# Performance work log

Measured on AMD Instinct MI355X. Metric: run time of the kernel, lower is better.

The kernel has to match this reference:

```python
import jax, jax.numpy as jnp
import numpy as np

NUM_NODES = 100_000
NUM_EDGES = 3_200_000
THETA = 1.0  # module hyperparameter (default 1.0)


def setup_inputs() -> dict:
    key = jax.random.key(0)
    k_v, k_src, k_dst, k_t1, k_t2, k_r = jax.random.split(key, 6)
    v = jax.random.normal(k_v, (NUM_NODES,), dtype=jnp.float32)
    src = jax.random.randint(k_src, (NUM_EDGES,), 0, NUM_NODES, dtype=jnp.int32)
    dst = jax.random.randint(k_dst, (NUM_EDGES,), 0, NUM_NODES, dtype=jnp.int32)
    theta_sd_1 = jax.random.normal(k_t1, (NUM_EDGES,), dtype=jnp.float32) * 0.1
    theta_sd_2 = jax.random.normal(k_t2, (NUM_EDGES,), dtype=jnp.float32) * 0.1
    # conductance = 1/resistance, resistance in (0.5, 2.0) -> conductance in (0.5, 2.0)
    conductance = 1.0 / jax.random.uniform(k_r, (NUM_EDGES,), dtype=jnp.float32, minval=0.5, maxval=2.0)
    return {"t": 0, "v": v, "src": src, "dst": dst,
            "theta_sd_1": theta_sd_1, "theta_sd_2": theta_sd_2,
            "conductance": conductance}


def reference(t, v, src, dst, theta_sd_1, theta_sd_2, conductance):
    # per-edge gated current: g(vs, vd) = relu(theta1*(vs - vd) + theta2)
    diff = v[src] - v[dst]                                   # [E]
    current = conductance * jax.nn.relu(theta_sd_1 * diff + theta_sd_2)  # [E]
    incoming = jax.ops.segment_sum(current, dst, num_segments=NUM_NODES)  # [N]
    outgoing = jax.ops.segment_sum(current, src, num_segments=NUM_NODES)  # [N]
    return (incoming - outgoing) / THETA
```

## Files before the change

kernel.cpp:

```cpp
#include <hip/hip_runtime.h>


#define RANGE   16384
#define P1_BLK  512

__global__ __launch_bounds__(256) void edge_current_kernel(
    const float* __restrict__ v,
    const int*   __restrict__ src,
    const int*   __restrict__ dst,
    const float* __restrict__ t1,
    const float* __restrict__ t2,
    const float* __restrict__ cond,
    float*       __restrict__ cur,
    int E)
{
    const int E4 = E & ~3;
    int i = (blockIdx.x * blockDim.x + threadIdx.x) * 4;
    int stride = gridDim.x * blockDim.x * 4;
    for (; i < E4; i += stride) {
        int4   s4 = *(const int4*)  (src  + i);
        int4   d4 = *(const int4*)  (dst  + i);
        float4 a4 = *(const float4*)(t1   + i);
        float4 b4 = *(const float4*)(t2   + i);
        float4 c4 = *(const float4*)(cond + i);
        float4 o;
        float x0 = fmaf(a4.x, v[s4.x] - v[d4.x], b4.x);
        float x1 = fmaf(a4.y, v[s4.y] - v[d4.y], b4.y);
        float x2 = fmaf(a4.z, v[s4.z] - v[d4.z], b4.z);
        float x3 = fmaf(a4.w, v[s4.w] - v[d4.w], b4.w);
        o.x = x0 > 0.0f ? c4.x * x0 : 0.0f;
        o.y = x1 > 0.0f ? c4.y * x1 : 0.0f;
        o.z = x2 > 0.0f ? c4.z * x2 : 0.0f;
        o.w = x3 > 0.0f ? c4.w * x3 : 0.0f;
        *(float4*)(cur + i) = o;
    }
    int t = E4 + blockIdx.x * blockDim.x + threadIdx.x;
    if (t < E) {
        float x = fmaf(t1[t], v[src[t]] - v[dst[t]], t2[t]);
        cur[t] = x > 0.0f ? cond[t] * x : 0.0f;
    }
}

__global__ __launch_bounds__(P1_BLK) void range_accum_kernel(
    const int*   __restrict__ src,
    const int*   __restrict__ dst,
    const float* __restrict__ cur,
    float*       __restrict__ partial,
    int N, int E, int B, int sliceLen)
{
    __shared__ __align__(16) float acc[RANGE];

    const int b    = blockIdx.x % B;
    const int r    = blockIdx.x / B;
    const int base = r * RANGE;
    const int len  = min(RANGE, N - base);

    for (int i = threadIdx.x; i < RANGE; i += P1_BLK) acc[i] = 0.0f;
    __syncthreads();

    const int E4 = E & ~3;
    const int s0 = b * sliceLen;
    const int s1 = min(s0 + sliceLen, E4);

    for (int i = s0 + threadIdx.x * 4; i < s1; i += P1_BLK * 4) {
        int4   ss = *(const int4*)  (src + i);
        int4   dd = *(const int4*)  (dst + i);
        float4 cc = *(const float4*)(cur + i);
        #define PROC(S, D, C)                                              \
            if ((C) != 0.0f) {                                             \
                unsigned du = (unsigned)((D) - base);                      \
                if (du < (unsigned)len) atomicAdd(&acc[du],  (C));         \
                unsigned su = (unsigned)((S) - base);                      \
                if (su < (unsigned)len) atomicAdd(&acc[su], -(C));         \
            }
        PROC(ss.x, dd.x, cc.x)
        PROC(ss.y, dd.y, cc.y)
        PROC(ss.z, dd.z, cc.z)
        PROC(ss.w, dd.w, cc.w)
    }
    if (b == B - 1) {
        for (int i = E4 + threadIdx.x; i < E; i += P1_BLK) {
            float c = cur[i];
            PROC(src[i], dst[i], c)
        }
        #undef PROC
    }

    __syncthreads();
    float* outp = partial + (size_t)b * N + base;
    const int len4 = len & ~3;
    for (int i = threadIdx.x * 4; i < len4; i += P1_BLK * 4)
        *(float4*)(outp + i) = *(const float4*)&acc[i];
    for (int i = len4 + threadIdx.x; i < len; i += P1_BLK)
        outp[i] = acc[i];
}

__global__ __launch_bounds__(256) void reduce_kernel(
    const float* __restrict__ partial, float* __restrict__ out, int N4, int B)
{
    int n = blockIdx.x * blockDim.x + threadIdx.x;
    if (n < N4) {
        float4 s = make_float4(0.f, 0.f, 0.f, 0.f);
        for (int p = 0; p < B; ++p) {
            float4 q = ((const float4*)partial)[(size_t)p * N4 + n];
            s.x += q.x; s.y += q.y; s.z += q.z; s.w += q.w;
        }
        ((float4*)out)[n] = s;
    }
}

__global__ __launch_bounds__(256) void atomic_fallback_kernel(
    const float* __restrict__ v, const int* __restrict__ src, const int* __restrict__ dst,
    const float* __restrict__ t1, const float* __restrict__ t2, const float* __restrict__ cond,
    float* __restrict__ out, int E)
{
    int i = blockIdx.x * blockDim.x + threadIdx.x;
    int stride = gridDim.x * blockDim.x;
    for (; i < E; i += stride) {
        int s = src[i], d = dst[i];
        float x = fmaf(t1[i], v[s] - v[d], t2[i]);
        if (x > 0.0f) {
            float c = cond[i] * x;
            atomicAdd(&out[d], c);
            atomicAdd(&out[s], -c);
        }
    }
}

extern "C" void kernel_launch(void* const* d_in, const int* in_sizes, int n_in,
                              void* d_out, int out_size, void* d_ws, size_t ws_size,
                              hipStream_t stream) {
    const float* v    = (const float*)d_in[1];
    const int*   src  = (const int*)  d_in[2];
    const int*   dst  = (const int*)  d_in[3];
    const float* t1   = (const float*)d_in[4];
    const float* t2   = (const float*)d_in[5];
    const float* cond = (const float*)d_in[6];
    float* out = (float*)d_out;
    const int E = in_sizes[2];
    const int N = out_size;

    const size_t curBytes = (((size_t)E * sizeof(float)) + 255) & ~(size_t)255;
    const size_t perCopy  = (size_t)N * sizeof(float);

    int B = 0;
    const int cands[] = {64, 48, 32, 24, 16, 12, 8};
    for (int c : cands) {
        if (curBytes + (size_t)c * perCopy <= ws_size) { B = c; break; }
    }

    if (B > 0 && (N & 3) == 0) {
        float* cur     = (float*)d_ws;
        float* partial = (float*)((char*)d_ws + curBytes);

        const int E4 = E & ~3;
        int chunks = (E4 + 3) / 4;
        int g0 = (chunks + 255) / 256;
        if (g0 < 1) g0 = 1;
        edge_current_kernel<<<g0, 256, 0, stream>>>(v, src, dst, t1, t2, cond, cur, E);

        const int R = (N + RANGE - 1) / RANGE;
        int sliceLen = ((E4 + B - 1) / B + 3) & ~3;
        range_accum_kernel<<<R * B, P1_BLK, 0, stream>>>(src, dst, cur, partial,
                                                         N, E, B, sliceLen);

        int n4 = N / 4;
        reduce_kernel<<<(n4 + 255) / 256, 256, 0, stream>>>(partial, out, n4, B);
    } else {
        hipMemsetAsync(out, 0, perCopy, stream);
        int grid = (E + 255) / 256;
        if (grid > 2048) grid = 2048;
        atomic_fallback_kernel<<<grid, 256, 0, stream>>>(v, src, dst, t1, t2, cond, out, E);
    }
}
```

Measured before the change: 85.64 us.

## Store per-edge currents in fp16 and enlarge LDS ranges and blocks

The per-edge current buffer is now written and read as fp16, halving that intermediate's traffic. The shared-memory accumulation range is doubled to 32768 nodes with 1024-thread blocks, which cuts how many times the src/dst arrays are re-scanned. Block ordering in the accumulation kernel is changed, the edge kernel processes 8 edges per thread with a capped grid, and a scalar reduce path is added for N not divisible by 4. fp16 storage of currents loses precision and may exceed the tolerance.

```diff
diff --git a/kernel.cpp b/kernel.cpp
--- a/kernel.cpp
+++ b/kernel.cpp
@@ -1,57 +1,85 @@
 #include <hip/hip_runtime.h>
-
-
-#define RANGE   16384
-#define P1_BLK  512
-
-__global__ __launch_bounds__(256) void edge_current_kernel(
+#include <hip/hip_fp16.h>
+
+
+#define RANGE   32768
+#define P1_BLK  1024
+#define P0_BLK  256
+
+__global__ __launch_bounds__(P0_BLK) void edge_current_kernel(
     const float* __restrict__ v,
     const int*   __restrict__ src,
     const int*   __restrict__ dst,
     const float* __restrict__ t1,
     const float* __restrict__ t2,
     const float* __restrict__ cond,
-    float*       __restrict__ cur,
+    __half*      __restrict__ cur,
     int E)
 {
-    const int E4 = E & ~3;
-    int i = (blockIdx.x * blockDim.x + threadIdx.x) * 4;
-    int stride = gridDim.x * blockDim.x * 4;
-    for (; i < E4; i += stride) {
-        int4   s4 = *(const int4*)  (src  + i);
-        int4   d4 = *(const int4*)  (dst  + i);
-        float4 a4 = *(const float4*)(t1   + i);
-        float4 b4 = *(const float4*)(t2   + i);
-        float4 c4 = *(const float4*)(cond + i);
-        float4 o;
-        float x0 = fmaf(a4.x, v[s4.x] - v[d4.x], b4.x);
-        float x1 = fmaf(a4.y, v[s4.y] - v[d4.y], b4.y);
-        float x2 = fmaf(a4.z, v[s4.z] - v[d4.z], b4.z);
-        float x3 = fmaf(a4.w, v[s4.w] - v[d4.w], b4.w);
-        o.x = x0 > 0.0f ? c4.x * x0 : 0.0f;
-        o.y = x1 > 0.0f ? c4.y * x1 : 0.0f;
-        o.z = x2 > 0.0f ? c4.z * x2 : 0.0f;
-        o.w = x3 > 0.0f ? c4.w * x3 : 0.0f;
-        *(float4*)(cur + i) = o;
-    }
-    int t = E4 + blockIdx.x * blockDim.x + threadIdx.x;
-    if (t < E) {
+    const int E8 = E & ~7;
+    const int tid = blockIdx.x * blockDim.x + threadIdx.x;
+    const int nthreads = gridDim.x * blockDim.x;
+
+    for (int i = tid * 8; i < E8; i += nthreads * 8) {
+        int4   sa = *(const int4*)  (src  + i);
+        int4   sb = *(const int4*)  (src  + i + 4);
+        int4   da = *(const int4*)  (dst  + i);
+        int4   db = *(const int4*)  (dst  + i + 4);
+        float4 aa = *(const float4*)(t1   + i);
+        float4 ab = *(const float4*)(t1   + i + 4);
+        float4 ba = *(const float4*)(t2   + i);
+        float4 bb = *(const float4*)(t2   + i + 4);
+        float4 ca = *(const float4*)(cond + i);
+        float4 cb = *(const float4*)(cond + i + 4);
+
+        float vs0 = v[sa.x], vs1 = v[sa.y], vs2 = v[sa.z], vs3 = v[sa.w];
+        float vs4 = v[sb.x], vs5 = v[sb.y], vs6 = v[sb.z], vs7 = v[sb.w];
+        float vd0 = v[da.x], vd1 = v[da.y], vd2 = v[da.z], vd3 = v[da.w];
+        float vd4 = v[db.x], vd5 = v[db.y], vd6 = v[db.z], vd7 = v[db.w];
+
+        float x0 = fmaf(aa.x, vs0 - vd0, ba.x);
+        float x1 = fmaf(aa.y, vs1 - vd1, ba.y);
+        float x2 = fmaf(aa.z, vs2 - vd2, ba.z);
+        float x3 = fmaf(aa.w, vs3 - vd3, ba.w);
+        float x4 = fmaf(ab.x, vs4 - vd4, bb.x);
+        float x5 = fmaf(ab.y, vs5 - vd5, bb.y);
+        float x6 = fmaf(ab.z, vs6 - vd6, bb.z);
+        float x7 = fmaf(ab.w, vs7 - vd7, bb.w);
+
+        float c0 = x0 > 0.0f ? ca.x * x0 : 0.0f;
+        float c1 = x1 > 0.0f ? ca.y * x1 : 0.0f;
+        float c2 = x2 > 0.0f ? ca.z * x2 : 0.0f;
+        float c3 = x3 > 0.0f ? ca.w * x3 : 0.0f;
+        float c4 = x4 > 0.0f ? cb.x * x4 : 0.0f;
+        float c5 = x5 > 0.0f ? cb.y * x5 : 0.0f;
+        float c6 = x6 > 0.0f ? cb.z * x6 : 0.0f;
+        float c7 = x7 > 0.0f ? cb.w * x7 : 0.0f;
+
+        union { __half2 h[4]; float4 f; } u;
+        u.h[0] = __floats2half2_rn(c0, c1);
+        u.h[1] = __floats2half2_rn(c2, c3);
+        u.h[2] = __floats2half2_rn(c4, c5);
+        u.h[3] = __floats2half2_rn(c6, c7);
+        *(float4*)(cur + i) = u.f;
+    }
+
+    for (int t = E8 + tid; t < E; t += nthreads) {
         float x = fmaf(t1[t], v[src[t]] - v[dst[t]], t2[t]);
-        cur[t] = x > 0.0f ? cond[t] * x : 0.0f;
+        cur[t] = __float2half(x > 0.0f ? cond[t] * x : 0.0f);
     }
 }
 
 __global__ __launch_bounds__(P1_BLK) void range_accum_kernel(
-    const int*   __restrict__ src,
-    const int*   __restrict__ dst,
-    const float* __restrict__ cur,
-    float*       __restrict__ partial,
-    int N, int E, int B, int sliceLen)
+    const int*    __restrict__ src,
+    const int*    __restrict__ dst,
+    const __half* __restrict__ cur,
+    float*        __restrict__ partial,
+    int N, int E, int B, int R, int sliceLen)
 {
     __shared__ __align__(16) float acc[RANGE];
 
-    const int b    = blockIdx.x % B;
-    const int r    = blockIdx.x / B;
+    const int r    = blockIdx.x % R;
+    const int b    = blockIdx.x / R;
     const int base = r * RANGE;
     const int len  = min(RANGE, N - base);
 
@@ -62,36 +90,41 @@
     const int s0 = b * sliceLen;
     const int s1 = min(s0 + sliceLen, E4);
 
-    for (int i = s0 + threadIdx.x * 4; i < s1; i += P1_BLK * 4) {
-        int4   ss = *(const int4*)  (src + i);
-        int4   dd = *(const int4*)  (dst + i);
-        float4 cc = *(const float4*)(cur + i);
-        #define PROC(S, D, C)                                              \
-            if ((C) != 0.0f) {                                             \
-                unsigned du = (unsigned)((D) - base);                      \
-                if (du < (unsigned)len) atomicAdd(&acc[du],  (C));         \
-                unsigned su = (unsigned)((S) - base);                      \
-                if (su < (unsigned)len) atomicAdd(&acc[su], -(C));         \
-            }
-        PROC(ss.x, dd.x, cc.x)
-        PROC(ss.y, dd.y, cc.y)
-        PROC(ss.z, dd.z, cc.z)
-        PROC(ss.w, dd.w, cc.w)
+    #define PROC(S, D, C)                                          \
+        if ((C) != 0.0f) {                                         \
+            unsigned du = (unsigned)((D) - base);                  \
+            if (du < (unsigned)len) atomicAdd(&acc[du],  (C));     \
+            unsigned su = (unsigned)((S) - base);                  \
+            if (su < (unsigned)len) atomicAdd(&acc[su], -(C));     \
+        }
+
+    for (int i = s0 + (int)threadIdx.x * 4; i < s1; i += P1_BLK * 4) {
+        int4    ss = *(const int4*)   (src + i);
+        int4    dd = *(const int4*)   (dst + i);
+        ushort4 hh = *(const ushort4*)(cur + i);
+        float c0 = __half2float(__ushort_as_half(hh.x));
+        float c1 = __half2float(__ushort_as_half(hh.y));
+        float c2 = __half2float(__ushort_as_half(hh.z));
+        float c3 = __half2float(__ushort_as_half(hh.w));
+        PROC(ss.x, dd.x, c0)
+        PROC(ss.y, dd.y, c1)
+        PROC(ss.z, dd.z, c2)
+        PROC(ss.w, dd.w, c3)
     }
     if (b == B - 1) {
-        for (int i = E4 + threadIdx.x; i < E; i += P1_BLK) {
-            float c = cur[i];
+        for (int i = E4 + (int)threadIdx.x; i < E; i += P1_BLK) {
+            float c = __half2float(cur[i]);
             PROC(src[i], dst[i], c)
         }
-        #undef PROC
-    }
+    }
+    #undef PROC
 
     __syncthreads();
     float* outp = partial + (size_t)b * N + base;
     const int len4 = len & ~3;
-    for (int i = threadIdx.x * 4; i < len4; i += P1_BLK * 4)
+    for (int i = (int)threadIdx.x * 4; i < len4; i += P1_BLK * 4)
         *(float4*)(outp + i) = *(const float4*)&acc[i];
-    for (int i = len4 + threadIdx.x; i < len; i += P1_BLK)
+    for (int i = len4 + (int)threadIdx.x; i < len; i += P1_BLK)
         outp[i] = acc[i];
 }
 
@@ -106,6 +139,17 @@
             s.x += q.x; s.y += q.y; s.z += q.z; s.w += q.w;
         }
         ((float4*)out)[n] = s;
+    }
+}
+
+__global__ __launch_bounds__(256) void reduce_scalar_kernel(
+    const float* __restrict__ partial, float* __restrict__ out, int N, int B)
+{
+    int n = blockIdx.x * blockDim.x + threadIdx.x;
+    if (n < N) {
+        float s = 0.0f;
+        for (int p = 0; p < B; ++p) s += partial[(size_t)p * N + n];
+        out[n] = s;
     }
 }
 
@@ -140,32 +184,37 @@
     const int E = in_sizes[2];
     const int N = out_size;
 
-    const size_t curBytes = (((size_t)E * sizeof(float)) + 255) & ~(size_t)255;
+    const size_t curBytes = (((size_t)E * sizeof(__half)) + 255) & ~(size_t)255;
     const size_t perCopy  = (size_t)N * sizeof(float);
 
     int B = 0;
-    const int cands[] = {64, 48, 32, 24, 16, 12, 8};
+    const int cands[] = {64, 48, 32, 16, 8};
     for (int c : cands) {
         if (curBytes + (size_t)c * perCopy <= ws_size) { B = c; break; }
     }
 
-    if (B > 0 && (N & 3) == 0) {
-        float* cur     = (float*)d_ws;
+    if (B > 0) {
+        __half* cur    = (__half*)d_ws;
         float* partial = (float*)((char*)d_ws + curBytes);
 
+        int chunks8 = (E + 7) / 8;
+        int g0 = (chunks8 + P0_BLK - 1) / P0_BLK;
+        if (g0 > 2048) g0 = 2048;
+        if (g0 < 1) g0 = 1;
+        edge_current_kernel<<<g0, P0_BLK, 0, stream>>>(v, src, dst, t1, t2, cond, cur, E);
+
+        const int R = (N + RANGE - 1) / RANGE;
         const int E4 = E & ~3;
-        int chunks = (E4 + 3) / 4;
-        int g0 = (chunks + 255) / 256;
-        if (g0 < 1) g0 = 1;
-        edge_current_kernel<<<g0, 256, 0, stream>>>(v, src, dst, t1, t2, cond, cur, E);
-
-        const int R = (N + RANGE - 1) / RANGE;
-        int sliceLen = ((E4 + B - 1) / B + 3) & ~3;
+        int sliceLen = (((E4 + B - 1) / B) + 3) & ~3;
         range_accum_kernel<<<R * B, P1_BLK, 0, stream>>>(src, dst, cur, partial,
-                                                         N, E, B, sliceLen);
-
-        int n4 = N / 4;
-        reduce_kernel<<<(n4 + 255) / 256, 256, 0, stream>>>(partial, out, n4, B);
+                                                         N, E, B, R, sliceLen);
+
+        if ((N & 3) == 0) {
+            int n4 = N / 4;
+            reduce_kernel<<<(n4 + 255) / 256, 256, 0, stream>>>(partial, out, n4, B);
+        } else {
+            reduce_scalar_kernel<<<(N + 255) / 256, 256, 0, stream>>>(partial, out, N, B);
+        }
     } else {
         hipMemsetAsync(out, 0, perCopy, stream);
         int grid = (E + 255) / 256;
```

Measured after the change: 86.91 us. Within noise of the previous version (+1.5%).
